# Performance work log

Measured on AMD Instinct MI355X. Metric: run time of the kernel, lower is better.

Reference implementation:

```python
import jax, jax.numpy as jnp
import numpy as np

B, N, S, D, H = 64, 4096, 8, 256, 512
ITERS = 3
EPS = 1e-8      # slot-attention renormalize epsilon
LN_EPS = 1e-5   # torch LayerNorm default


def _ln(x, g, b):
    m = jnp.mean(x, -1, keepdims=True)
    v = jnp.mean((x - m) ** 2, -1, keepdims=True)
    return (x - m) * jax.lax.rsqrt(v + LN_EPS) * g + b


def setup_inputs() -> dict:
    key = jax.random.key(0)
    ks = jax.random.split(key, 12)

    def xav(k, shape):
        s = (6.0 / (shape[-2] + shape[-1])) ** 0.5
        return jax.random.uniform(k, shape, jnp.float32, -s, s)

    gru_s = 1.0 / (D ** 0.5)
    return {
        "inputs": jax.random.normal(ks[0], (B, N, D), jnp.float32),
        "init_noise": jax.random.normal(ks[1], (B, S, D), jnp.float32),
        "slots_mu": xav(ks[2], (1, 1, D)),
        "slots_log_sigma": xav(ks[3], (1, 1, D)),
        "ln_in_g": jnp.ones(D), "ln_in_b": jnp.zeros(D),
        "ln_slots_g": jnp.ones(D), "ln_slots_b": jnp.zeros(D),
        "ln_mlp_g": jnp.ones(D), "ln_mlp_b": jnp.zeros(D),
        "Wq": xav(ks[4], (D, D)),
        "Wk": xav(ks[5], (D, D)),
        "Wv": xav(ks[6], (D, D)),
        "W_ih": jax.random.uniform(ks[7], (3 * D, D), jnp.float32, -gru_s, gru_s),
        "W_hh": jax.random.uniform(ks[8], (3 * D, D), jnp.float32, -gru_s, gru_s),
        "b_ih": jnp.zeros(3 * D), "b_hh": jnp.zeros(3 * D),
        "W1": xav(ks[9], (H, D)), "b1": jnp.zeros(H),
        "W2": xav(ks[10], (D, H)), "b2": jnp.zeros(D),
    }


def reference(inputs, init_noise, slots_mu, slots_log_sigma,
              ln_in_g, ln_in_b, ln_slots_g, ln_slots_b, ln_mlp_g, ln_mlp_b,
              Wq, Wk, Wv, W_ih, W_hh, b_ih, b_hh, W1, b1, W2, b2):
    x = _ln(inputs, ln_in_g, ln_in_b)               # (B,N,D)
    k = jnp.einsum('bnd,ed->bne', x, Wk)             # (B,N,D)
    v = jnp.einsum('bnd,ed->bne', x, Wv)             # (B,N,D)
    slots = slots_mu + jnp.exp(slots_log_sigma) * init_noise  # (B,S,D)
    scale = D ** (-0.5)
    for _ in range(ITERS):
        prev = slots
        s = _ln(slots, ln_slots_g, ln_slots_b)
        q = jnp.einsum('bsd,ed->bse', s, Wq) * scale
        logits = jnp.einsum('bse,bne->bsn', q, k)    # (B,S,N)
        attn = jax.nn.softmax(logits, -1) + EPS
        attn = attn / jnp.sum(attn, -1, keepdims=True)
        upd = jnp.einsum('bsn,bne->bse', attn, v)    # (B,S,D)
        # GRUCell (torch semantics)
        gx = jnp.einsum('bsd,ed->bse', upd, W_ih) + b_ih
        gh = jnp.einsum('bsd,ed->bse', prev, W_hh) + b_hh
        xr, xz, xn = jnp.split(gx, 3, -1)
        hr, hz, hn = jnp.split(gh, 3, -1)
        r = jax.nn.sigmoid(xr + hr)
        z = jax.nn.sigmoid(xz + hz)
        n = jnp.tanh(xn + r * hn)
        slots = (1.0 - z) * n + z * prev
        # residual MLP
        m = _ln(slots, ln_mlp_g, ln_mlp_b)
        h1 = jax.nn.relu(jnp.einsum('bsd,hd->bsh', m, W1) + b1)
        slots = slots + jnp.einsum('bsh,dh->bsd', h1, W2) + b2
    return slots
```

## Files before the change

### kernel.cpp

```cpp
#include <hip/hip_runtime.h>

#define BB 64
#define NN 4096
#define SS 8
#define DD 256
#define HH 512
#define NCH 8
#define CHK 512
#define LSP 516
#define XSTR 520

typedef __attribute__((ext_vector_type(4))) float f32x4;
typedef __attribute__((ext_vector_type(8))) short short8;
typedef __attribute__((ext_vector_type(8))) __bf16 bf16x8;

static __device__ __forceinline__ f32x4 MFMA(short8 a, short8 b, f32x4 c){
  return __builtin_amdgcn_mfma_f32_16x16x32_bf16(
      __builtin_bit_cast(bf16x8, a), __builtin_bit_cast(bf16x8, b), c, 0, 0, 0);
}

static __device__ __forceinline__ unsigned short f2bf(float f){
  unsigned int x = __builtin_bit_cast(unsigned int, f);
  x += 0x7FFFu + ((x >> 16) & 1u);
  return (unsigned short)(x >> 16);
}

static __device__ __forceinline__ unsigned int pk2(float a, float b){
  return (unsigned int)f2bf(a) | ((unsigned int)f2bf(b) << 16);
}

__global__ __launch_bounds__(256, 4) void wqkT_kernel(
    const float* __restrict__ Wq, const float* __restrict__ Wk, float* __restrict__ out)
{
  __shared__ float sh[256];
  const int d2 = blockIdx.x, t = threadIdx.x;
  sh[t] = Wk[(size_t)t * 256 + d2];
  __syncthreads();
  float acc = 0.f;
  #pragma unroll 8
  for(int e = 0; e < 256; ++e) acc += sh[e] * Wq[(size_t)e * 256 + t];
  out[(size_t)d2 * 256 + t] = acc * 0.0625f;
}

__global__ __launch_bounds__(256, 4) void m_kernel(
    const float* __restrict__ Wih, const float* __restrict__ Wv, float* __restrict__ out)
{
  __shared__ float sh[256];
  const int e = blockIdx.x, t = threadIdx.x;
  sh[t] = Wih[(size_t)e * 256 + t];
  __syncthreads();
  float acc = 0.f;
  #pragma unroll 8
  for(int d = 0; d < 256; ++d) acc += sh[d] * Wv[(size_t)d * 256 + t];
  out[(size_t)e * 256 + t] = acc;
}

struct PackDesc {
  const float* src[7];
  unsigned short* dst[7];
  int ET[7];
  int K[7];
  int blkStart[8];
};

__global__ void pack_all_kernel(PackDesc pd){
  int blk = blockIdx.x;
  int seg = 0;
  #pragma unroll
  for(int i = 1; i < 7; ++i) if(blk >= pd.blkStart[i]) seg = i;
  int tid = (blk - pd.blkStart[seg]) * 256 + threadIdx.x;
  int ET = pd.ET[seg], K = pd.K[seg];
  if(tid >= ET * 16 * K) return;
  int i    = tid & 7;
  int lane = (tid >> 3) & 63;
  int rest = tid >> 9;
  int et = rest % ET;
  int kk = rest / ET;
  int row = et * 16 + (lane & 15);
  int col = kk * 32 + ((lane >> 4) << 3) + i;
  pd.dst[seg][tid] = f2bf(pd.src[seg][(size_t)row * K + col]);
}

__global__ __launch_bounds__(256, 4) void ln_kernel(
    const float* __restrict__ inp, const float* __restrict__ g, const float* __restrict__ bta,
    unsigned short* __restrict__ x, unsigned short* __restrict__ xT)
{
  __shared__ char xs[64 * XSTR];
  const int t = threadIdx.x, w = t >> 6, l = t & 63;
  const size_t row0 = (size_t)blockIdx.x * 64;
  const int b = (int)(row0 >> 12);
  const int n_base = (int)(row0 & 4095);
  const int li = l & 15, lg = l >> 4;

  float4 gg[4], bb[4];
  #pragma unroll
  for(int q = 0; q < 4; ++q){
    gg[q] = ((const float4*)g)[li + q * 16];
    bb[q] = ((const float4*)bta)[li + q * 16];
  }
  #pragma unroll
  for(int rr = 0; rr < 4; ++rr){
    int r = w * 16 + rr * 4 + lg;
    const float4* rp = (const float4*)(inp + (row0 + r) * DD);
    float4 xv[4];
    #pragma unroll
    for(int q = 0; q < 4; ++q) xv[q] = rp[li + q * 16];
    float s1 = 0.f, s2 = 0.f;
    #pragma unroll
    for(int q = 0; q < 4; ++q){
      s1 += xv[q].x + xv[q].y + xv[q].z + xv[q].w;
      s2 += xv[q].x*xv[q].x + xv[q].y*xv[q].y + xv[q].z*xv[q].z + xv[q].w*xv[q].w;
    }
    #pragma unroll
    for(int o = 8; o >= 1; o >>= 1){ s1 += __shfl_xor(s1, o); s2 += __shfl_xor(s2, o); }
    float mean = s1 * (1.0f/256.0f);
    float inv  = rsqrtf(s2 * (1.0f/256.0f) - mean*mean + 1e-5f);
    #pragma unroll
    for(int q = 0; q < 4; ++q){
      float y0 = (xv[q].x-mean)*inv*gg[q].x + bb[q].x;
      float y1 = (xv[q].y-mean)*inv*gg[q].y + bb[q].y;
      float y2 = (xv[q].z-mean)*inv*gg[q].z + bb[q].z;
      float y3 = (xv[q].w-mean)*inv*gg[q].w + bb[q].w;
      uint2 pv = make_uint2(pk2(y0,y1), pk2(y2,y3));
      *(uint2*)((char*)x + (row0 + r) * 512 + q * 128 + li * 8) = pv;
      *(uint2*)(xs + r * XSTR + ((q * 128 + li * 8) ^ ((r & 7) << 4))) = pv;
    }
  }
  __syncthreads();

  const int dl = t >> 3, nv = t & 7;
  #pragma unroll
  for(int p = 0; p < 8; ++p){
    int d = p * 32 + dl;
    unsigned int u[4];
    #pragma unroll
    for(int jj = 0; jj < 4; ++jj){
      int n0 = nv * 8 + jj * 2;
      unsigned int lo = *(unsigned short*)(xs + n0 * XSTR + ((d * 2) ^ ((n0 & 7) << 4)));
      int n1 = n0 + 1;
      unsigned int hi = *(unsigned short*)(xs + n1 * XSTR + ((d * 2) ^ ((n1 & 7) << 4)));
      u[jj] = lo | (hi << 16);
    }
    uint4 vv = make_uint4(u[0], u[1], u[2], u[3]);
    *(uint4*)(xT + (((size_t)(b * 256 + d)) << 12) + n_base + nv * 8) = vv;
  }
}

__global__ __launch_bounds__(256, 1) void init_kernel(
    const float* __restrict__ noise, const float* __restrict__ mu, const float* __restrict__ lsg,
    const float* __restrict__ lng, const float* __restrict__ lnb,
    const short8* __restrict__ wqkp, float* __restrict__ slots, float* __restrict__ qbuf)
{
  const int b = blockIdx.x, t = threadIdx.x, w = t >> 6, l = t & 63;
  __shared__ float SLN[SS * DD];
  __shared__ unsigned short A1[16 * DD];
  float muv = mu[t];
  float sgv = __expf(lsg[t]);
  #pragma unroll
  for(int s = 0; s < SS; ++s){
    float v = muv + sgv * noise[(size_t)b * 2048 + s * 256 + t];
    slots[(size_t)b * 2048 + s * 256 + t] = v;
    SLN[s * 256 + t] = v;
  }
  __syncthreads();
  float4 g4 = ((const float4*)lng)[l], bb4 = ((const float4*)lnb)[l];
  for(int sh = 0; sh < 2; ++sh){
    int s = w * 2 + sh;
    float4 x4 = ((const float4*)(SLN + s * 256))[l];
    float s1 = x4.x + x4.y + x4.z + x4.w;
    float s2 = x4.x*x4.x + x4.y*x4.y + x4.z*x4.z + x4.w*x4.w;
    #pragma unroll
    for(int o = 32; o >= 1; o >>= 1){ s1 += __shfl_xor(s1, o); s2 += __shfl_xor(s2, o); }
    float mean = s1 * (1.0f/256.0f);
    float inv  = rsqrtf(s2 * (1.0f/256.0f) - mean*mean + 1e-5f);
    float y0 = (x4.x-mean)*inv*g4.x + bb4.x;
    float y1 = (x4.y-mean)*inv*g4.y + bb4.y;
    float y2 = (x4.z-mean)*inv*g4.z + bb4.z;
    float y3 = (x4.w-mean)*inv*g4.w + bb4.w;
    int byte = s * 512 + ((l * 8) ^ ((s & 7) << 4));
    *(uint2*)((char*)A1 + byte) = make_uint2(pk2(y0,y1), pk2(y2,y3));
  }
  __syncthreads();
  const int m = l & 15;
  short8 af[8];
  #pragma unroll
  for(int kk = 0; kk < 8; ++kk){
    int ab = m * 512 + (((kk * 64) + ((l >> 4) << 4)) ^ ((m & 7) << 4));
    af[kk] = *(const short8*)((const char*)A1 + ab);
  }
  #pragma unroll
  for(int i = 0; i < 4; ++i){
    int et = w + i * 4;
    f32x4 c = (f32x4){0,0,0,0};
    #pragma unroll
    for(int kk = 0; kk < 8; ++kk) c = MFMA(af[kk], wqkp[((kk * 16 + et) << 6) + l], c);
    int e = et * 16 + (l & 15);
    #pragma unroll
    for(int j = 0; j < 4; ++j){
      int s = ((l >> 4) << 2) + j;
      if(s < 8) qbuf[(size_t)b * 2048 + s * 256 + e] = c[j];
    }
  }
}

__global__ __launch_bounds__(256, 3) void attn_kernel(
    const unsigned short* __restrict__ x_, const unsigned short* __restrict__ xT_,
    const float* __restrict__ qbuf, float* __restrict__ pupd, float* __restrict__ pms)
{
  const int blk = blockIdx.x;
  const int b = blk >> 3, c = blk & 7;
  const int t = threadIdx.x, w = t >> 6, l = t & 63;
  __shared__ float ls[8 * LSP];

  const int m = l & 15;
  short8 aq[8];
  #pragma unroll
  for(int kk = 0; kk < 8; ++kk){
    if(m < 8){
      const float* qp = qbuf + (size_t)b * 2048 + m * 256 + kk * 32 + ((l >> 4) << 3);
      float4 qa = *(const float4*)qp;
      float4 qb = *(const float4*)(qp + 4);
      int4 pv = make_int4((int)pk2(qa.x,qa.y), (int)pk2(qa.z,qa.w),
                          (int)pk2(qb.x,qb.y), (int)pk2(qb.z,qb.w));
      aq[kk] = __builtin_bit_cast(short8, pv);
    } else {
      aq[kk] = (short8){0,0,0,0,0,0,0,0};
    }
  }

  const unsigned short* xb = x_ + ((size_t)b * NN + (size_t)c * CHK) * DD;
  #pragma unroll
  for(int nt = 0; nt < 8; ++nt){
    int nb = w * 128 + nt * 16;
    f32x4 acc = (f32x4){0,0,0,0};
    #pragma unroll
    for(int kk = 0; kk < 8; ++kk){
      short8 bk = *(const short8*)(xb + (size_t)(nb + m) * DD + kk * 32 + ((l >> 4) << 3));
      acc = MFMA(aq[kk], bk, acc);
    }
    if(l < 32){
      int s4 = (l >> 4) * 4;
      #pragma unroll
      for(int j = 0; j < 4; ++j) ls[(s4 + j) * LSP + nb + m] = acc[j];
    }
  }
  __syncthreads();

  for(int sh = 0; sh < 2; ++sh){
    int s = w * 2 + sh;
    float* base = ls + s * LSP;
    float4 v0 = *(float4*)(base + l * 4);
    float4 v1 = *(float4*)(base + 256 + l * 4);
    float mx = fmaxf(fmaxf(fmaxf(v0.x,v0.y),fmaxf(v0.z,v0.w)),
                     fmaxf(fmaxf(v1.x,v1.y),fmaxf(v1.z,v1.w)));
    #pragma unroll
    for(int o = 32; o >= 1; o >>= 1) mx = fmaxf(mx, __shfl_xor(mx, o));
    float e0 = __expf(v0.x-mx), e1 = __expf(v0.y-mx), e2 = __expf(v0.z-mx), e3 = __expf(v0.w-mx);
    float e4 = __expf(v1.x-mx), e5 = __expf(v1.y-mx), e6 = __expf(v1.z-mx), e7 = __expf(v1.w-mx);
    float sm = e0+e1+e2+e3+e4+e5+e6+e7;
    #pragma unroll
    for(int o = 32; o >= 1; o >>= 1) sm += __shfl_xor(sm, o);
    *(float4*)(base + l * 4)       = make_float4(e0,e1,e2,e3);
    *(float4*)(base + 256 + l * 4) = make_float4(e4,e5,e6,e7);
    if(l == 0){
      pms[(((size_t)b * 8 + c) * 8 + s) * 2    ] = mx;
      pms[(((size_t)b * 8 + c) * 8 + s) * 2 + 1] = sm;
    }
  }
  __syncthreads();

  short8 pa[16];
  #pragma unroll
  for(int kk = 0; kk < 16; ++kk){
    if(m < 8){
      const float* pp = ls + m * LSP + kk * 32 + ((l >> 4) << 3);
      int4 pv = make_int4((int)pk2(pp[0],pp[1]), (int)pk2(pp[2],pp[3]),
                          (int)pk2(pp[4],pp[5]), (int)pk2(pp[6],pp[7]));
      pa[kk] = __builtin_bit_cast(short8, pv);
    } else {
      pa[kk] = (short8){0,0,0,0,0,0,0,0};
    }
  }

  const unsigned short* xt = xT_ + ((size_t)b << 20) + (size_t)c * CHK;
  #pragma unroll
  for(int dt = 0; dt < 4; ++dt){
    int d0 = w * 64 + dt * 16;
    f32x4 acc = (f32x4){0,0,0,0};
    #pragma unroll
    for(int kk = 0; kk < 16; ++kk){
      short8 bv = *(const short8*)(xt + ((size_t)(d0 + m) << 12) + kk * 32 + ((l >> 4) << 3));
      acc = MFMA(pa[kk], bv, acc);
    }
    if(l < 32){
      int s4 = (l >> 4) * 4;
      #pragma unroll
      for(int j = 0; j < 4; ++j)
        pupd[((size_t)b * 8 + c) * 2048 + (s4 + j) * 256 + d0 + m] = acc[j];
    }
  }
}

__global__ __launch_bounds__(1024, 1) void update_kernel(
    const float* __restrict__ pupd, const float* __restrict__ pms,
    float* __restrict__ slots, float* __restrict__ qbuf,
    const short8* __restrict__ mp, const short8* __restrict__ whh,
    const float* __restrict__ bih, const float* __restrict__ bhh,
    const short8* __restrict__ w1p, const float* __restrict__ b1v,
    const short8* __restrict__ w2p, const float* __restrict__ b2v,
    const float* __restrict__ lnsg, const float* __restrict__ lnsb,
    const float* __restrict__ lnmg, const float* __restrict__ lnmb,
    const short8* __restrict__ wqkp,
    float* __restrict__ dout, const int last)
{
  const int b = blockIdx.x, t = threadIdx.x, w = t >> 6, l = t & 63;
  __shared__ unsigned short A1[16 * 256];
  __shared__ unsigned short A2[16 * 256];
  __shared__ unsigned short A3[16 * 512];
  __shared__ float GR[8 * 256], GZ[8 * 256], GXN[8 * 256], GHN[8 * 256];
  __shared__ float SL[8 * 256];
  __shared__ float PMS[128];

  if(t < 128) PMS[t] = pms[(size_t)b * 128 + t];
  __syncthreads();

  const int col = t & 255, sg = t >> 8;
  float upd[2], pv[2];
  #pragma unroll
  for(int ss = 0; ss < 2; ++ss){
    int s = sg * 2 + ss;
    float mx = -1e30f;
    #pragma unroll
    for(int cc = 0; cc < 8; ++cc) mx = fmaxf(mx, PMS[(cc * 8 + s) * 2]);
    float Z = 0.f, u = 0.f;
    #pragma unroll
    for(int cc = 0; cc < 8; ++cc){
      float e = __expf(PMS[(cc * 8 + s) * 2] - mx);
      Z += e * PMS[(cc * 8 + s) * 2 + 1];
      u += e * pupd[((size_t)b * 8 + cc) * 2048 + s * 256 + col];
    }
    upd[ss] = u / Z;
    pv[ss]  = slots[(size_t)b * 2048 + s * 256 + col];
  }
  #pragma unroll
  for(int ss = 0; ss < 2; ++ss){
    int s = sg * 2 + ss;
    int byte = s * 512 + ((col * 2) ^ ((s & 7) << 4));
    *(unsigned short*)((char*)A1 + byte) = f2bf(upd[ss]);
    *(unsigned short*)((char*)A2 + byte) = f2bf(pv[ss]);
  }
  __syncthreads();

  {
    const int m = l & 15;
    short8 a1f[8], a2f[8];
    #pragma unroll
    for(int kk = 0; kk < 8; ++kk){
      int ab = m * 512 + (((kk * 64) + ((l >> 4) << 4)) ^ ((m & 7) << 4));
      a1f[kk] = *(const short8*)((const char*)A1 + ab);
      a2f[kk] = *(const short8*)((const char*)A2 + ab);
    }
    #pragma unroll
    for(int i = 0; i < 3; ++i){
      int et = w + i * 16;
      f32x4 c1 = (f32x4){0,0,0,0}, c2 = (f32x4){0,0,0,0};
      #pragma unroll
      for(int kk = 0; kk < 8; ++kk){
        c1 = MFMA(a1f[kk], mp[((kk * 48 + et) << 6) + l], c1);
        c2 = MFMA(a2f[kk], whh[((kk * 48 + et) << 6) + l], c2);
      }
      int e = et * 16 + (l & 15);
      float xb = bih[e], hb = bhh[e];
      #pragma unroll
      for(int j = 0; j < 4; ++j){
        int s = ((l >> 4) << 2) + j;
        if(s < 8){
          float xx = c1[j] + xb, h = c2[j] + hb;
          if(i == 0)      GR[s * 256 + e      ] = 1.f/(1.f + __expf(-(xx + h)));
          else if(i == 1) GZ[s * 256 + (e-256)] = 1.f/(1.f + __expf(-(xx + h)));
          else { GXN[s * 256 + (e-512)] = xx; GHN[s * 256 + (e-512)] = h; }
        }
      }
    }
  }
  __syncthreads();

  #pragma unroll
  for(int ss = 0; ss < 2; ++ss){
    int s = sg * 2 + ss, idx = s * 256 + col;
    float r = GR[idx], z = GZ[idx], xn = GXN[idx], hn = GHN[idx];
    float nn = tanhf(xn + r * hn);
    SL[idx] = (1.f - z) * nn + z * pv[ss];
  }
  __syncthreads();

  if(w < 8){
    float4 g4 = ((const float4*)lnmg)[l], bb4 = ((const float4*)lnmb)[l];
    int s = w;
    float4 x4 = ((const float4*)(SL + s * 256))[l];
    float s1 = x4.x + x4.y + x4.z + x4.w;
    float s2 = x4.x*x4.x + x4.y*x4.y + x4.z*x4.z + x4.w*x4.w;
    #pragma unroll
    for(int o = 32; o >= 1; o >>= 1){ s1 += __shfl_xor(s1, o); s2 += __shfl_xor(s2, o); }
    float mean = s1 * (1.0f/256.0f);
    float inv  = rsqrtf(s2 * (1.0f/256.0f) - mean*mean + 1e-5f);
    float y0 = (x4.x-mean)*inv*g4.x + bb4.x;
    float y1 = (x4.y-mean)*inv*g4.y + bb4.y;
    float y2 = (x4.z-mean)*inv*g4.z + bb4.z;
    float y3 = (x4.w-mean)*inv*g4.w + bb4.w;
    int byte = s * 512 + ((l * 8) ^ ((s & 7) << 4));
    *(uint2*)((char*)A1 + byte) = make_uint2(pk2(y0,y1), pk2(y2,y3));
  }
  __syncthreads();

  {
    const int m = l & 15;
    short8 af[8];
    #pragma unroll
    for(int kk = 0; kk < 8; ++kk){
      int ab = m * 512 + (((kk * 64) + ((l >> 4) << 4)) ^ ((m & 7) << 4));
      af[kk] = *(const short8*)((const char*)A1 + ab);
    }
    #pragma unroll
    for(int i = 0; i < 2; ++i){
      int et = w + i * 16;
      f32x4 c = (f32x4){0,0,0,0};
      #pragma unroll
      for(int kk = 0; kk < 8; ++kk) c = MFMA(af[kk], w1p[((kk * 32 + et) << 6) + l], c);
      int e = et * 16 + (l & 15);
      float bb = b1v[e];
      #pragma unroll
      for(int j = 0; j < 4; ++j){
        int s = ((l >> 4) << 2) + j;
        if(s < 8){
          float h = fmaxf(c[j] + bb, 0.f);
          int byte = s * 1024 + ((e * 2) ^ ((s & 7) << 4));
          *(unsigned short*)((char*)A3 + byte) = f2bf(h);
        }
      }
    }
  }
  __syncthreads();

  {
    const int m = l & 15;
    short8 af[16];
    #pragma unroll
    for(int kk = 0; kk < 16; ++kk){
      int ab = m * 1024 + (((kk * 64) + ((l >> 4) << 4)) ^ ((m & 7) << 4));
      af[kk] = *(const short8*)((const char*)A3 + ab);
    }
    {
      int et = w;
      f32x4 c = (f32x4){0,0,0,0};
      #pragma unroll
      for(int kk = 0; kk < 16; ++kk) c = MFMA(af[kk], w2p[((kk * 16 + et) << 6) + l], c);
      int e = et * 16 + (l & 15);
      float bb = b2v[e];
      #pragma unroll
      for(int j = 0; j < 4; ++j){
        int s = ((l >> 4) << 2) + j;
        if(s < 8) GR[s * 256 + e] = SL[s * 256 + e] + c[j] + bb;
      }
    }
  }
  __syncthreads();

  for(int i = t; i < 2048; i += 1024){
    float v = GR[i];
    slots[(size_t)b * 2048 + i] = v;
    if(last) dout[(size_t)b * 2048 + i] = v;
  }
  if(w < 8){
    float4 g4 = ((const float4*)lnsg)[l], bb4 = ((const float4*)lnsb)[l];
    int s = w;
    float4 x4 = ((const float4*)(GR + s * 256))[l];
    float s1 = x4.x + x4.y + x4.z + x4.w;
    float s2 = x4.x*x4.x + x4.y*x4.y + x4.z*x4.z + x4.w*x4.w;
    #pragma unroll
    for(int o = 32; o >= 1; o >>= 1){ s1 += __shfl_xor(s1, o); s2 += __shfl_xor(s2, o); }
    float mean = s1 * (1.0f/256.0f);
    float inv  = rsqrtf(s2 * (1.0f/256.0f) - mean*mean + 1e-5f);
    float y0 = (x4.x-mean)*inv*g4.x + bb4.x;
    float y1 = (x4.y-mean)*inv*g4.y + bb4.y;
    float y2 = (x4.z-mean)*inv*g4.z + bb4.z;
    float y3 = (x4.w-mean)*inv*g4.w + bb4.w;
    int byte = s * 512 + ((l * 8) ^ ((s & 7) << 4));
    *(uint2*)((char*)A1 + byte) = make_uint2(pk2(y0,y1), pk2(y2,y3));
  }
  __syncthreads();
  {
    const int m = l & 15;
    short8 af[8];
    #pragma unroll
    for(int kk = 0; kk < 8; ++kk){
      int ab = m * 512 + (((kk * 64) + ((l >> 4) << 4)) ^ ((m & 7) << 4));
      af[kk] = *(const short8*)((const char*)A1 + ab);
    }
    {
      int et = w;
      f32x4 c = (f32x4){0,0,0,0};
      #pragma unroll
      for(int kk = 0; kk < 8; ++kk) c = MFMA(af[kk], wqkp[((kk * 16 + et) << 6) + l], c);
      int e = et * 16 + (l & 15);
      #pragma unroll
      for(int j = 0; j < 4; ++j){
        int s = ((l >> 4) << 2) + j;
        if(s < 8) qbuf[(size_t)b * 2048 + s * 256 + e] = c[j];
      }
    }
  }
}

extern "C" void kernel_launch(void* const* d_in, const int* in_sizes, int n_in,
                              void* d_out, int out_size, void* d_ws, size_t ws_size,
                              hipStream_t stream)
{
  const float* inp   = (const float*)d_in[0];
  const float* noise = (const float*)d_in[1];
  const float* mu    = (const float*)d_in[2];
  const float* lsg   = (const float*)d_in[3];
  const float* lngi  = (const float*)d_in[4];
  const float* lnbi  = (const float*)d_in[5];
  const float* lngs  = (const float*)d_in[6];
  const float* lnbs  = (const float*)d_in[7];
  const float* lngm  = (const float*)d_in[8];
  const float* lnbm  = (const float*)d_in[9];
  const float* Wq    = (const float*)d_in[10];
  const float* Wk    = (const float*)d_in[11];
  const float* Wv    = (const float*)d_in[12];
  const float* Wih   = (const float*)d_in[13];
  const float* Whh   = (const float*)d_in[14];
  const float* bih   = (const float*)d_in[15];
  const float* bhh   = (const float*)d_in[16];
  const float* W1    = (const float*)d_in[17];
  const float* b1    = (const float*)d_in[18];
  const float* W2    = (const float*)d_in[19];
  const float* b2    = (const float*)d_in[20];
  float* dout = (float*)d_out;

  char* ws = (char*)d_ws;
  size_t off = 0;
  unsigned short* x   = (unsigned short*)(ws + off); off += (size_t)BB*NN*DD*2;
  unsigned short* xT  = (unsigned short*)(ws + off); off += (size_t)BB*NN*DD*2;
  short8* wqkp= (short8*)(ws + off); off += (size_t)256*256*2;
  short8* mp  = (short8*)(ws + off); off += (size_t)768*256*2;
  short8* whhp= (short8*)(ws + off); off += (size_t)768*256*2;
  short8* w1p = (short8*)(ws + off); off += (size_t)512*256*2;
  short8* w2p = (short8*)(ws + off); off += (size_t)256*512*2;
  float* wqkT = (float*)(ws + off);  off += (size_t)256*256*4;
  float* mf32 = (float*)(ws + off);  off += (size_t)768*256*4;
  float* qbuf = (float*)(ws + off);  off += (size_t)512*256*4;
  float* slots= (float*)(ws + off);  off += (size_t)512*256*4;
  float* pupd = (float*)(ws + off);  off += (size_t)64*8*8*256*4;
  float* pms  = (float*)(ws + off);  off += (size_t)64*8*8*2*4;

  wqkT_kernel<<<256, 256, 0, stream>>>(Wq, Wk, wqkT);
  m_kernel<<<768, 256, 0, stream>>>(Wih, Wv, mf32);

  PackDesc pd;
  const float* srcs[7] = {wqkT, mf32, Whh, W1, W2, Wq, Wq};
  unsigned short* dsts[7] = {(unsigned short*)wqkp, (unsigned short*)mp,
                             (unsigned short*)whhp, (unsigned short*)w1p,
                             (unsigned short*)w2p, 0, 0};
  int ets[7] = {16, 48, 48, 32, 16, 0, 0};
  int ks [7] = {256, 256, 256, 256, 512, 0, 0};
  int cum = 0;
  for(int i = 0; i < 7; ++i){
    pd.src[i] = srcs[i]; pd.dst[i] = dsts[i]; pd.ET[i] = ets[i]; pd.K[i] = ks[i];
    pd.blkStart[i] = cum;
    cum += (ets[i] * 16 * ks[i] + 255) / 256;
  }
  pd.blkStart[7] = cum;
  pack_all_kernel<<<cum, 256, 0, stream>>>(pd);

  ln_kernel<<<4096, 256, 0, stream>>>(inp, lngi, lnbi, x, xT);
  init_kernel<<<64, 256, 0, stream>>>(noise, mu, lsg, lngs, lnbs, wqkp, slots, qbuf);

  for(int it = 0; it < 3; ++it){
    attn_kernel<<<512, 256, 0, stream>>>(x, xT, qbuf, pupd, pms);
    update_kernel<<<64, 1024, 0, stream>>>(pupd, pms, slots, qbuf, mp, whhp,
        bih, bhh, w1p, b1, w2p, b2, lngs, lnbs, lngm, lnbm, wqkp, dout, (it == 2) ? 1 : 0);
  }
}
```

Measured before the change: 405.0 us.

## Drop global transposed x copy; transpose x tiles in LDS inside attention

The layernorm kernel no longer writes a second transposed bf16 copy of x (64x4096x256), which removes one full-size global write from setup. The attention kernel instead reads its x chunk row-major, transposes 64-row groups into a swizzled LDS buffer, and runs the attn-times-V MFMAs from LDS. This trades a large one-time write for extra LDS traffic and barriers in each of the three attention iterations. The attention kernel already reads the same chunk for the logits, so the second read may hit cache, but the 32KB of added shared memory could lower occupancy.

```diff
diff --git a/kernel.cpp b/kernel.cpp
--- a/kernel.cpp
+++ b/kernel.cpp
@@ -8,7 +8,6 @@
 #define NCH 8
 #define CHK 512
 #define LSP 516
-#define XSTR 520
 
 typedef __attribute__((ext_vector_type(4))) float f32x4;
 typedef __attribute__((ext_vector_type(8))) short short8;
@@ -56,18 +55,18 @@
 }
 
 struct PackDesc {
-  const float* src[7];
-  unsigned short* dst[7];
-  int ET[7];
-  int K[7];
-  int blkStart[8];
+  const float* src[5];
+  unsigned short* dst[5];
+  int ET[5];
+  int K[5];
+  int blkStart[6];
 };
 
 __global__ void pack_all_kernel(PackDesc pd){
   int blk = blockIdx.x;
   int seg = 0;
   #pragma unroll
-  for(int i = 1; i < 7; ++i) if(blk >= pd.blkStart[i]) seg = i;
+  for(int i = 1; i < 5; ++i) if(blk >= pd.blkStart[i]) seg = i;
   int tid = (blk - pd.blkStart[seg]) * 256 + threadIdx.x;
   int ET = pd.ET[seg], K = pd.K[seg];
   if(tid >= ET * 16 * K) return;
@@ -83,13 +82,10 @@
 
 __global__ __launch_bounds__(256, 4) void ln_kernel(
     const float* __restrict__ inp, const float* __restrict__ g, const float* __restrict__ bta,
-    unsigned short* __restrict__ x, unsigned short* __restrict__ xT)
-{
-  __shared__ char xs[64 * XSTR];
+    unsigned short* __restrict__ x)
+{
   const int t = threadIdx.x, w = t >> 6, l = t & 63;
   const size_t row0 = (size_t)blockIdx.x * 64;
-  const int b = (int)(row0 >> 12);
-  const int n_base = (int)(row0 & 4095);
   const int li = l & 15, lg = l >> 4;
 
   float4 gg[4], bb[4];
@@ -121,28 +117,9 @@
       float y1 = (xv[q].y-mean)*inv*gg[q].y + bb[q].y;
       float y2 = (xv[q].z-mean)*inv*gg[q].z + bb[q].z;
       float y3 = (xv[q].w-mean)*inv*gg[q].w + bb[q].w;
-      uint2 pv = make_uint2(pk2(y0,y1), pk2(y2,y3));
-      *(uint2*)((char*)x + (row0 + r) * 512 + q * 128 + li * 8) = pv;
-      *(uint2*)(xs + r * XSTR + ((q * 128 + li * 8) ^ ((r & 7) << 4))) = pv;
-    }
-  }
-  __syncthreads();
-
-  const int dl = t >> 3, nv = t & 7;
-  #pragma unroll
-  for(int p = 0; p < 8; ++p){
-    int d = p * 32 + dl;
-    unsigned int u[4];
-    #pragma unroll
-    for(int jj = 0; jj < 4; ++jj){
-      int n0 = nv * 8 + jj * 2;
-      unsigned int lo = *(unsigned short*)(xs + n0 * XSTR + ((d * 2) ^ ((n0 & 7) << 4)));
-      int n1 = n0 + 1;
-      unsigned int hi = *(unsigned short*)(xs + n1 * XSTR + ((d * 2) ^ ((n1 & 7) << 4)));
-      u[jj] = lo | (hi << 16);
-    }
-    uint4 vv = make_uint4(u[0], u[1], u[2], u[3]);
-    *(uint4*)(xT + (((size_t)(b * 256 + d)) << 12) + n_base + nv * 8) = vv;
+      *(uint2*)((char*)x + (row0 + r) * 512 + q * 128 + li * 8) =
+          make_uint2(pk2(y0,y1), pk2(y2,y3));
+    }
   }
 }
 
@@ -204,20 +181,21 @@
 }
 
 __global__ __launch_bounds__(256, 3) void attn_kernel(
-    const unsigned short* __restrict__ x_, const unsigned short* __restrict__ xT_,
-    const float* __restrict__ qbuf, float* __restrict__ pupd, float* __restrict__ pms)
+    const unsigned short* __restrict__ x_, const float* __restrict__ qbuf,
+    float* __restrict__ pupd, float* __restrict__ pms)
 {
   const int blk = blockIdx.x;
   const int b = blk >> 3, c = blk & 7;
   const int t = threadIdx.x, w = t >> 6, l = t & 63;
   __shared__ float ls[8 * LSP];
-
-  const int m = l & 15;
+  __shared__ __align__(16) char xv[256 * 128];
+
+  const int m = l & 15, lg = l >> 4;
   short8 aq[8];
   #pragma unroll
   for(int kk = 0; kk < 8; ++kk){
     if(m < 8){
-      const float* qp = qbuf + (size_t)b * 2048 + m * 256 + kk * 32 + ((l >> 4) << 3);
+      const float* qp = qbuf + (size_t)b * 2048 + m * 256 + kk * 32 + (lg << 3);
       float4 qa = *(const float4*)qp;
       float4 qb = *(const float4*)(qp + 4);
       int4 pv = make_int4((int)pk2(qa.x,qa.y), (int)pk2(qa.z,qa.w),
@@ -235,7 +213,7 @@
     f32x4 acc = (f32x4){0,0,0,0};
     #pragma unroll
     for(int kk = 0; kk < 8; ++kk){
-      short8 bk = *(const short8*)(xb + (size_t)(nb + m) * DD + kk * 32 + ((l >> 4) << 3));
+      short8 bk = *(const short8*)(xb + (size_t)(nb + m) * DD + kk * 32 + (lg << 3));
       acc = MFMA(aq[kk], bk, acc);
     }
     if(l < 32){
@@ -273,7 +251,7 @@
   #pragma unroll
   for(int kk = 0; kk < 16; ++kk){
     if(m < 8){
-      const float* pp = ls + m * LSP + kk * 32 + ((l >> 4) << 3);
+      const float* pp = ls + m * LSP + kk * 32 + (lg << 3);
       int4 pv = make_int4((int)pk2(pp[0],pp[1]), (int)pk2(pp[2],pp[3]),
                           (int)pk2(pp[4],pp[5]), (int)pk2(pp[6],pp[7]));
       pa[kk] = __builtin_bit_cast(short8, pv);
@@ -282,21 +260,53 @@
     }
   }
 
-  const unsigned short* xt = xT_ + ((size_t)b << 20) + (size_t)c * CHK;
-  #pragma unroll
-  for(int dt = 0; dt < 4; ++dt){
-    int d0 = w * 64 + dt * 16;
-    f32x4 acc = (f32x4){0,0,0,0};
-    #pragma unroll
-    for(int kk = 0; kk < 16; ++kk){
-      short8 bv = *(const short8*)(xt + ((size_t)(d0 + m) << 12) + kk * 32 + ((l >> 4) << 3));
-      acc = MFMA(pa[kk], bv, acc);
-    }
-    if(l < 32){
-      int s4 = (l >> 4) * 4;
+  f32x4 acc[4];
+  #pragma unroll
+  for(int dt = 0; dt < 4; ++dt) acc[dt] = (f32x4){0,0,0,0};
+  const int p = t & 31, db = t >> 5;
+  for(int ng = 0; ng < 8; ++ng){
+    if(ng) __syncthreads();
+    {
+      const unsigned short* rA = xb + (size_t)(ng * 64 + 2 * p) * DD + db * 32;
+      const unsigned short* rB = rA + DD;
+      #pragma unroll
+      for(int q = 0; q < 4; ++q){
+        uint4 va = *(const uint4*)(rA + q * 8);
+        uint4 vb = *(const uint4*)(rB + q * 8);
+        unsigned int wa[4] = {va.x, va.y, va.z, va.w};
+        unsigned int wb[4] = {vb.x, vb.y, vb.z, vb.w};
+        #pragma unroll
+        for(int h = 0; h < 4; ++h){
+          int d0 = db * 32 + q * 8 + h * 2;
+          unsigned int a = wa[h], bv = wb[h];
+          unsigned int v0 = (a & 0xFFFFu) | (bv << 16);
+          unsigned int v1 = (a >> 16) | (bv & 0xFFFF0000u);
+          *(unsigned int*)(xv + d0 * 128 + ((p * 4) ^ ((d0 & 7) << 4))) = v0;
+          int d1 = d0 + 1;
+          *(unsigned int*)(xv + d1 * 128 + ((p * 4) ^ ((d1 & 7) << 4))) = v1;
+        }
+      }
+    }
+    __syncthreads();
+    #pragma unroll
+    for(int kkloc = 0; kkloc < 2; ++kkloc){
+      int kk = ng * 2 + kkloc;
+      #pragma unroll
+      for(int dt = 0; dt < 4; ++dt){
+        int d = w * 64 + dt * 16 + m;
+        short8 bv = *(const short8*)(xv + d * 128 + ((kkloc * 64 + lg * 16) ^ ((d & 7) << 4)));
+        acc[dt] = MFMA(pa[kk], bv, acc[dt]);
+      }
+    }
+  }
+  if(l < 32){
+    int s4 = (l >> 4) * 4;
+    #pragma unroll
+    for(int dt = 0; dt < 4; ++dt){
+      int d0 = w * 64 + dt * 16;
       #pragma unroll
       for(int j = 0; j < 4; ++j)
-        pupd[((size_t)b * 8 + c) * 2048 + (s4 + j) * 256 + d0 + m] = acc[j];
+        pupd[((size_t)b * 8 + c) * 2048 + (s4 + j) * 256 + d0 + m] = acc[dt][j];
     }
   }
 }
@@ -542,7 +552,6 @@
   char* ws = (char*)d_ws;
   size_t off = 0;
   unsigned short* x   = (unsigned short*)(ws + off); off += (size_t)BB*NN*DD*2;
-  unsigned short* xT  = (unsigned short*)(ws + off); off += (size_t)BB*NN*DD*2;
   short8* wqkp= (short8*)(ws + off); off += (size_t)256*256*2;
   short8* mp  = (short8*)(ws + off); off += (size_t)768*256*2;
   short8* whhp= (short8*)(ws + off); off += (size_t)768*256*2;
@@ -559,26 +568,26 @@
   m_kernel<<<768, 256, 0, stream>>>(Wih, Wv, mf32);
 
   PackDesc pd;
-  const float* srcs[7] = {wqkT, mf32, Whh, W1, W2, Wq, Wq};
-  unsigned short* dsts[7] = {(unsigned short*)wqkp, (unsigned short*)mp,
+  const float* srcs[5] = {wqkT, mf32, Whh, W1, W2};
+  unsigned short* dsts[5] = {(unsigned short*)wqkp, (unsigned short*)mp,
                              (unsigned short*)whhp, (unsigned short*)w1p,
-                             (unsigned short*)w2p, 0, 0};
-  int ets[7] = {16, 48, 48, 32, 16, 0, 0};
-  int ks [7] = {256, 256, 256, 256, 512, 0, 0};
+                             (unsigned short*)w2p};
+  int ets[5] = {16, 48, 48, 32, 16};
+  int ks [5] = {256, 256, 256, 256, 512};
   int cum = 0;
-  for(int i = 0; i < 7; ++i){
+  for(int i = 0; i < 5; ++i){
     pd.src[i] = srcs[i]; pd.dst[i] = dsts[i]; pd.ET[i] = ets[i]; pd.K[i] = ks[i];
     pd.blkStart[i] = cum;
     cum += (ets[i] * 16 * ks[i] + 255) / 256;
   }
-  pd.blkStart[7] = cum;
+  pd.blkStart[5] = cum;
   pack_all_kernel<<<cum, 256, 0, stream>>>(pd);
 
-  ln_kernel<<<4096, 256, 0, stream>>>(inp, lngi, lnbi, x, xT);
+  ln_kernel<<<4096, 256, 0, stream>>>(inp, lngi, lnbi, x);
   init_kernel<<<64, 256, 0, stream>>>(noise, mu, lsg, lngs, lnbs, wqkp, slots, qbuf);
 
   for(int it = 0; it < 3; ++it){
-    attn_kernel<<<512, 256, 0, stream>>>(x, xT, qbuf, pupd, pms);
+    attn_kernel<<<512, 256, 0, stream>>>(x, qbuf, pupd, pms);
     update_kernel<<<64, 1024, 0, stream>>>(pupd, pms, slots, qbuf, mp, whhp,
         bih, bhh, w1p, b1, w2p, b2, lngs, lnbs, lngm, lnbm, wqkp, dout, (it == 2) ? 1 : 0);
   }
```

After: 366.3 us. 9.6% less time.
